# Kernel optimization log

Measured on AMD Instinct MI355X. Metric: run time of the kernel, lower is better.

Reference implementation:

```python
import jax, jax.numpy as jnp
import numpy as np

DT = 0.1
ROUTER_BLOCKS = 64
REPEAT = 64
IN_SIZE = 2048
HIDDEN = 4096
NNZ_W = int(IN_SIZE * HIDDEN * 0.01)   # 83886
NNZ_R = int(HIDDEN * HIDDEN * 0.01)    # 167772
BATCH = 512


def sparse_linear(x, rows, cols, vals, bias, out_features):
    """Edge-list sparse matmul: out[b, cols[e]] += x[b, rows[e]] * vals[e].
    Equivalent to torch.addmm(bias, x, W_csr) with W built from COO (coalesce
    sums duplicates; scatter-add does the same)."""
    contrib = x[:, rows] * vals  # [B, nnz]
    out = jnp.zeros((x.shape[0], out_features), x.dtype).at[:, cols].add(contrib)
    return out + bias


def setup_inputs() -> dict:
    key = jax.random.key(0)
    ks = jax.random.split(key, 20)
    inp = {}
    inp["x"] = jax.random.normal(ks[0], (BATCH, IN_SIZE), jnp.float32)
    inp["h_prev"] = jax.random.normal(ks[1], (BATCH, HIDDEN), jnp.float32)
    inp["gate"] = jax.random.uniform(ks[2], (BATCH, 1), jnp.float32)
    # SparseLinear params (init scale 1/sqrt(in_features), bias zeros)
    inp["W_vals"] = jax.random.normal(ks[3], (NNZ_W,), jnp.float32) / np.sqrt(IN_SIZE).astype(np.float32)
    inp["W_bias"] = jnp.zeros((HIDDEN,), jnp.float32)
    inp["R_vals"] = jax.random.normal(ks[4], (NNZ_R,), jnp.float32) / np.sqrt(HIDDEN).astype(np.float32)
    inp["R_bias"] = jnp.zeros((HIDDEN,), jnp.float32)
    inp["P_vals"] = jax.random.normal(ks[5], (NNZ_R,), jnp.float32) / np.sqrt(HIDDEN).astype(np.float32)
    inp["P_bias"] = jnp.zeros((HIDDEN,), jnp.float32)
    inp["router_w"] = jax.random.normal(ks[6], (ROUTER_BLOCKS, IN_SIZE), jnp.float32) / np.sqrt(IN_SIZE).astype(np.float32)
    inp["router_b"] = jnp.zeros((ROUTER_BLOCKS,), jnp.float32)
    # tau ~ U(0.1, 0.5) per TAU_CONCEPT_RANGE
    inp["tau"] = jax.random.uniform(ks[7], (HIDDEN,), jnp.float32) * 0.4 + 0.1
    # edge lists (int constants)
    inp["W_rows"] = jax.random.randint(ks[8], (NNZ_W,), 0, IN_SIZE, jnp.int32)
    inp["W_cols"] = jax.random.randint(ks[9], (NNZ_W,), 0, HIDDEN, jnp.int32)
    inp["R_rows"] = jax.random.randint(ks[10], (NNZ_R,), 0, HIDDEN, jnp.int32)
    inp["R_cols"] = jax.random.randint(ks[11], (NNZ_R,), 0, HIDDEN, jnp.int32)
    inp["P_rows"] = jax.random.randint(ks[12], (NNZ_R,), 0, HIDDEN, jnp.int32)
    inp["P_cols"] = jax.random.randint(ks[13], (NNZ_R,), 0, HIDDEN, jnp.int32)
    return inp


def reference(x, h_prev, gate, W_vals, W_bias, R_vals, R_bias, P_vals, P_bias,
              router_w, router_b, tau, W_rows, W_cols, R_rows, R_cols, P_rows, P_cols):
    r_gate = jax.nn.sigmoid(x @ router_w.T + router_b)            # [B, 64]
    mask = jnp.repeat(r_gate, REPEAT, axis=1)[:, :HIDDEN]          # [B, hidden]
    sensory = sparse_linear(x, W_rows, W_cols, W_vals, W_bias, HIDDEN) * mask
    rec = sparse_linear(h_prev, R_rows, R_cols, R_vals, R_bias, HIDDEN)
    target = jnp.tanh(sensory + rec)
    h_new = h_prev + gate * (target - h_prev) * (DT / tau)
    pred = sparse_linear(h_new, P_rows, P_cols, P_vals, P_bias, HIDDEN)
    return (h_new, pred)
```

## Files before the change

kernel.cpp:

```cpp
#include <hip/hip_runtime.h>
#include <math.h>

namespace {

constexpr int B     = 512;
constexpr int IN    = 2048;
constexpr int HID   = 4096;
constexpr int NNZ_W = 83886;
constexpr int NNZ_R = 167772;
constexpr int NTOT  = NNZ_W + 2 * NNZ_R;
constexpr int NCOLS = 3 * HID;
constexpr int SLOT  = 128;
constexpr float DT  = 0.1f;

struct ushort4_t { unsigned short x, y, z, w; };

__device__ __forceinline__ float bf2f(unsigned short u) {
  return __uint_as_float((unsigned int)u << 16);
}
__device__ __forceinline__ unsigned short f2bf(float f) {
  unsigned int u = __float_as_uint(f);
  u += 0x7FFFu + ((u >> 16) & 1u);
  return (unsigned short)(u >> 16);
}

__global__ void prep_k(const float* __restrict__ x, unsigned short* __restrict__ xTb,
                       const float* __restrict__ h, float* __restrict__ hT,
                       unsigned short* __restrict__ hTb,
                       const float* __restrict__ rw, const float* __restrict__ rb,
                       float* __restrict__ rgT, int* __restrict__ cnt) {
  __shared__ float sh[4 * IN];
  const int blk = blockIdx.x;
  const int tid = threadIdx.x;

  if (blk < 768) {
    const bool isX = blk < 256;
    const float* src; int C, tb;
    if (isX) { src = x; C = IN;  tb = blk; }
    else     { src = h; C = HID; tb = blk - 256; }
    const int tx_n = C / 64;
    const int bx = (tb % tx_n) * 64;
    const int by = (tb / tx_n) * 64;
    const int tx = tid & 63;
    const int ty = tid >> 6;
    for (int i = ty; i < 64; i += 8)
      sh[i * 65 + tx] = src[(size_t)(by + i) * C + bx + tx];
    __syncthreads();
    for (int i = ty; i < 64; i += 8) {
      const float v = sh[tx * 65 + i];
      const size_t di = (size_t)(bx + i) * B + by + tx;
      if (isX) xTb[di] = f2bf(v);
      else     { hT[di] = v; hTb[di] = f2bf(v); }
    }
  } else if (blk < 896) {
    const int b0 = (blk - 768) * 4;
    for (int k = tid; k < 4 * IN; k += 512) sh[k] = x[(size_t)b0 * IN + k];
    __syncthreads();
    const int wave = tid >> 6;
    const int lane = tid & 63;
#pragma unroll
    for (int j = 0; j < 8; ++j) {
      const int o = wave * 8 + j;
      const float* w = rw + (size_t)o * IN;
      float s0 = 0.f, s1 = 0.f, s2 = 0.f, s3 = 0.f;
      for (int i = 0; i < IN / 64; ++i) {
        const float wv = w[lane + 64 * i];
        s0 += sh[0 * IN + lane + 64 * i] * wv;
        s1 += sh[1 * IN + lane + 64 * i] * wv;
        s2 += sh[2 * IN + lane + 64 * i] * wv;
        s3 += sh[3 * IN + lane + 64 * i] * wv;
      }
#pragma unroll
      for (int d = 1; d < 64; d <<= 1) {
        s0 += __shfl_xor(s0, d);
        s1 += __shfl_xor(s1, d);
        s2 += __shfl_xor(s2, d);
        s3 += __shfl_xor(s3, d);
      }
      if (lane == 0) {
        const float bias = rb[o];
        rgT[o * B + b0 + 0] = 1.f / (1.f + expf(-(s0 + bias)));
        rgT[o * B + b0 + 1] = 1.f / (1.f + expf(-(s1 + bias)));
        rgT[o * B + b0 + 2] = 1.f / (1.f + expf(-(s2 + bias)));
        rgT[o * B + b0 + 3] = 1.f / (1.f + expf(-(s3 + bias)));
      }
    }
  } else {
    const int i = (blk - 896) * 512 + tid;
    if (i < NCOLS) cnt[i] = 0;
  }
}

__global__ void slotscat_k(const int* __restrict__ Wc, const int* __restrict__ Rc,
                           const int* __restrict__ Pc, const int* __restrict__ Wr,
                           const int* __restrict__ Rr, const int* __restrict__ Pr,
                           const float* __restrict__ Wv, const float* __restrict__ Rv,
                           const float* __restrict__ Pv, int* __restrict__ cnt,
                           float2* __restrict__ packed) {
  const int i = blockIdx.x * blockDim.x + threadIdx.x;
  if (i >= NTOT) return;
  int gc, r; float v;
  if (i < NNZ_W)              { gc = Wc[i];                 r = Wr[i]; v = Wv[i]; }
  else if (i < NNZ_W + NNZ_R) { int j = i - NNZ_W;          gc = HID + Rc[j];     r = Rr[j]; v = Rv[j]; }
  else                        { int j = i - NNZ_W - NNZ_R; gc = 2 * HID + Pc[j]; r = Pr[j]; v = Pv[j]; }
  const int p = atomicAdd(&cnt[gc], 1);
  packed[(size_t)gc * SLOT + p] = make_float2(v, __int_as_float(r));
}

__device__ __forceinline__ float4 gather_col_bf(const unsigned short* __restrict__ srcb,
                                                const float2* __restrict__ packed,
                                                int gc, int n, int boff, float bias) {
  float4 acc = make_float4(bias, bias, bias, bias);
  const float2* ep = packed + (size_t)gc * SLOT;
  int i = 0;
  for (; i + 8 <= n; i += 8) {
    float2 e[8]; ushort4_t s[8];
#pragma unroll
    for (int j = 0; j < 8; ++j) e[j] = ep[i + j];
#pragma unroll
    for (int j = 0; j < 8; ++j)
      s[j] = *(const ushort4_t*)(srcb + (size_t)__float_as_int(e[j].y) * B + boff);
#pragma unroll
    for (int j = 0; j < 8; ++j) {
      acc.x += e[j].x * bf2f(s[j].x);
      acc.y += e[j].x * bf2f(s[j].y);
      acc.z += e[j].x * bf2f(s[j].z);
      acc.w += e[j].x * bf2f(s[j].w);
    }
  }
  for (; i < n; ++i) {
    const float2 e = ep[i];
    const ushort4_t s = *(const ushort4_t*)(srcb + (size_t)__float_as_int(e.y) * B + boff);
    acc.x += e.x * bf2f(s.x);
    acc.y += e.x * bf2f(s.y);
    acc.z += e.x * bf2f(s.z);
    acc.w += e.x * bf2f(s.w);
  }
  return acc;
}

__device__ __forceinline__ void col_chunk(int blk, int wave, int& c, int& boff, int lane) {
  const int p = blk & 7;
  const int chunk = p >> 2;
  const int cgrp = ((p & 3) << 8) | (blk >> 3);
  c = cgrp * 4 + wave;
  boff = chunk * 256 + lane * 4;
}

__global__ void fused_gc_k(const unsigned short* __restrict__ xTb,
                           const unsigned short* __restrict__ hTb,
                           const float* __restrict__ hT,
                           const float2* __restrict__ packed, const int* __restrict__ cnt,
                           const float* __restrict__ rgT,
                           const float* __restrict__ gate, const float* __restrict__ tau,
                           const float* __restrict__ wb, const float* __restrict__ rb,
                           float* __restrict__ hnT, unsigned short* __restrict__ hnb) {
  int c, boff;
  col_chunk(blockIdx.x, threadIdx.x >> 6, c, boff, threadIdx.x & 63);

  const float4 sens = gather_col_bf(xTb, packed, c, cnt[c], boff, wb[c]);
  const float4 rec  = gather_col_bf(hTb, packed, HID + c, cnt[HID + c], boff, rb[c]);

  const float4 m  = *(const float4*)(rgT + (size_t)(c >> 6) * B + boff);
  const float4 g  = *(const float4*)(gate + boff);
  const float4 hp = *(const float4*)(hT + (size_t)c * B + boff);
  const float k = DT / tau[c];
  float4 hn;
  hn.x = hp.x + g.x * (tanhf(sens.x * m.x + rec.x) - hp.x) * k;
  hn.y = hp.y + g.y * (tanhf(sens.y * m.y + rec.y) - hp.y) * k;
  hn.z = hp.z + g.z * (tanhf(sens.z * m.z + rec.z) - hp.z) * k;
  hn.w = hp.w + g.w * (tanhf(sens.w * m.w + rec.w) - hp.w) * k;
  *(float4*)(hnT + (size_t)c * B + boff) = hn;
  ushort4_t hb;
  hb.x = f2bf(hn.x); hb.y = f2bf(hn.y); hb.z = f2bf(hn.z); hb.w = f2bf(hn.w);
  *(ushort4_t*)(hnb + (size_t)c * B + boff) = hb;
}

__global__ void pred_k(const unsigned short* __restrict__ hnb,
                       const float2* __restrict__ packed, const int* __restrict__ cnt,
                       const float* __restrict__ pb, float* __restrict__ predT) {
  int c, boff;
  col_chunk(blockIdx.x, threadIdx.x >> 6, c, boff, threadIdx.x & 63);
  const float4 p = gather_col_bf(hnb, packed, 2 * HID + c, cnt[2 * HID + c], boff, pb[c]);
  *(float4*)(predT + (size_t)c * B + boff) = p;
}

__global__ void transpose_out_k(const float* __restrict__ sA, float* __restrict__ dA,
                                int tilesA, const float* __restrict__ sB,
                                float* __restrict__ dB) {
  __shared__ float t[64][65];
  int tb = blockIdx.x;
  const float* src; float* dst;
  if (tb < tilesA) { src = sA; dst = dA; }
  else             { tb -= tilesA; src = sB; dst = dB; }
  const int tx_n = B / 64;
  const int bx = (tb % tx_n) * 64;
  const int by = (tb / tx_n) * 64;
  const int tx = threadIdx.x & 63;
  const int ty = threadIdx.x >> 6;
  for (int i = ty; i < 64; i += 8)
    t[i][tx] = src[(size_t)(by + i) * B + bx + tx];
  __syncthreads();
  for (int i = ty; i < 64; i += 8)
    dst[(size_t)(bx + i) * HID + by + tx] = t[tx][i];
}

}

extern "C" void kernel_launch(void* const* d_in, const int* in_sizes, int n_in,
                              void* d_out, int out_size, void* d_ws, size_t ws_size,
                              hipStream_t stream) {
  const float* x        = (const float*)d_in[0];
  const float* h_prev   = (const float*)d_in[1];
  const float* gate     = (const float*)d_in[2];
  const float* W_vals   = (const float*)d_in[3];
  const float* W_bias   = (const float*)d_in[4];
  const float* R_vals   = (const float*)d_in[5];
  const float* R_bias   = (const float*)d_in[6];
  const float* P_vals   = (const float*)d_in[7];
  const float* P_bias   = (const float*)d_in[8];
  const float* router_w = (const float*)d_in[9];
  const float* router_b = (const float*)d_in[10];
  const float* tau      = (const float*)d_in[11];
  const int* W_rows = (const int*)d_in[12];
  const int* W_cols = (const int*)d_in[13];
  const int* R_rows = (const int*)d_in[14];
  const int* R_cols = (const int*)d_in[15];
  const int* P_rows = (const int*)d_in[16];
  const int* P_cols = (const int*)d_in[17];

  float* ws = (float*)d_ws;
  unsigned short* xTb = (unsigned short*)ws;
  float*  hT     = ws + (size_t)IN * B / 2;
  unsigned short* hTb = (unsigned short*)(hT + (size_t)HID * B);
  float*  rgT    = (float*)(hTb + (size_t)HID * B);
  float*  hnT    = rgT + 64 * B;
  unsigned short* hnb = (unsigned short*)(hnT + (size_t)HID * B);
  float2* packed = (float2*)(hnb + (size_t)HID * B);
  int*    cnt    = (int*)(packed + (size_t)NCOLS * SLOT);
  float*  predT  = ws;

  float* out_h = (float*)d_out;
  float* out_p = out_h + (size_t)B * HID;

  prep_k<<<920, 512, 0, stream>>>(x, xTb, h_prev, hT, hTb,
                                  router_w, router_b, rgT, cnt);

  slotscat_k<<<(NTOT + 255) / 256, 256, 0, stream>>>(W_cols, R_cols, P_cols,
                                                     W_rows, R_rows, P_rows,
                                                     W_vals, R_vals, P_vals,
                                                     cnt, packed);

  fused_gc_k<<<2048, 256, 0, stream>>>(xTb, hTb, hT, packed, cnt, rgT,
                                       gate, tau, W_bias, R_bias, hnT, hnb);

  pred_k<<<2048, 256, 0, stream>>>(hnb, packed, cnt, P_bias, predT);

  transpose_out_k<<<1024, 512, 0, stream>>>(hnT, out_h, 512, predT, out_p);
}
```

Baseline: 114.8 us.

## Overlap h transpose with pred gather and use nontemporal loads/stores

Moves the output transpose of h_new into the pred gather kernel as extra blocks, so it runs alongside the pred sparse gather instead of after it. The pred transpose becomes its own small kernel. Streaming loads and stores throughout (index lists, packed edges, hT, hnT, outputs) are marked nontemporal to reduce cache pollution. Nontemporal hints on the packed edge list, which both gathers reuse, may cost cache hits.

```diff
diff --git a/kernel.cpp b/kernel.cpp
--- a/kernel.cpp
+++ b/kernel.cpp
@@ -12,6 +12,9 @@
 constexpr int NCOLS = 3 * HID;
 constexpr int SLOT  = 128;
 constexpr float DT  = 0.1f;
+
+typedef float f4 __attribute__((ext_vector_type(4)));
+typedef float f2 __attribute__((ext_vector_type(2)));
 
 struct ushort4_t { unsigned short x, y, z, w; };
 
@@ -44,13 +47,13 @@
     const int tx = tid & 63;
     const int ty = tid >> 6;
     for (int i = ty; i < 64; i += 8)
-      sh[i * 65 + tx] = src[(size_t)(by + i) * C + bx + tx];
+      sh[i * 65 + tx] = __builtin_nontemporal_load(&src[(size_t)(by + i) * C + bx + tx]);
     __syncthreads();
     for (int i = ty; i < 64; i += 8) {
       const float v = sh[tx * 65 + i];
       const size_t di = (size_t)(bx + i) * B + by + tx;
       if (isX) xTb[di] = f2bf(v);
-      else     { hT[di] = v; hTb[di] = f2bf(v); }
+      else     { __builtin_nontemporal_store(v, &hT[di]); hTb[di] = f2bf(v); }
     }
   } else if (blk < 896) {
     const int b0 = (blk - 768) * 4;
@@ -100,23 +103,36 @@
   const int i = blockIdx.x * blockDim.x + threadIdx.x;
   if (i >= NTOT) return;
   int gc, r; float v;
-  if (i < NNZ_W)              { gc = Wc[i];                 r = Wr[i]; v = Wv[i]; }
-  else if (i < NNZ_W + NNZ_R) { int j = i - NNZ_W;          gc = HID + Rc[j];     r = Rr[j]; v = Rv[j]; }
-  else                        { int j = i - NNZ_W - NNZ_R; gc = 2 * HID + Pc[j]; r = Pr[j]; v = Pv[j]; }
+  if (i < NNZ_W) {
+    gc = __builtin_nontemporal_load(&Wc[i]);
+    r  = __builtin_nontemporal_load(&Wr[i]);
+    v  = __builtin_nontemporal_load(&Wv[i]);
+  } else if (i < NNZ_W + NNZ_R) {
+    const int j = i - NNZ_W;
+    gc = HID + __builtin_nontemporal_load(&Rc[j]);
+    r  = __builtin_nontemporal_load(&Rr[j]);
+    v  = __builtin_nontemporal_load(&Rv[j]);
+  } else {
+    const int j = i - NNZ_W - NNZ_R;
+    gc = 2 * HID + __builtin_nontemporal_load(&Pc[j]);
+    r  = __builtin_nontemporal_load(&Pr[j]);
+    v  = __builtin_nontemporal_load(&Pv[j]);
+  }
   const int p = atomicAdd(&cnt[gc], 1);
-  packed[(size_t)gc * SLOT + p] = make_float2(v, __int_as_float(r));
-}
-
-__device__ __forceinline__ float4 gather_col_bf(const unsigned short* __restrict__ srcb,
-                                                const float2* __restrict__ packed,
-                                                int gc, int n, int boff, float bias) {
-  float4 acc = make_float4(bias, bias, bias, bias);
-  const float2* ep = packed + (size_t)gc * SLOT;
+  f2 e; e.x = v; e.y = __int_as_float(r);
+  __builtin_nontemporal_store(e, (f2*)&packed[(size_t)gc * SLOT + p]);
+}
+
+__device__ __forceinline__ f4 gather_col_bf(const unsigned short* __restrict__ srcb,
+                                            const float2* __restrict__ packed,
+                                            int gc, int n, int boff, float bias) {
+  f4 acc; acc.x = bias; acc.y = bias; acc.z = bias; acc.w = bias;
+  const f2* ep = (const f2*)(packed + (size_t)gc * SLOT);
   int i = 0;
   for (; i + 8 <= n; i += 8) {
-    float2 e[8]; ushort4_t s[8];
-#pragma unroll
-    for (int j = 0; j < 8; ++j) e[j] = ep[i + j];
+    f2 e[8]; ushort4_t s[8];
+#pragma unroll
+    for (int j = 0; j < 8; ++j) e[j] = __builtin_nontemporal_load(ep + i + j);
 #pragma unroll
     for (int j = 0; j < 8; ++j)
       s[j] = *(const ushort4_t*)(srcb + (size_t)__float_as_int(e[j].y) * B + boff);
@@ -129,7 +145,7 @@
     }
   }
   for (; i < n; ++i) {
-    const float2 e = ep[i];
+    const f2 e = __builtin_nontemporal_load(ep + i);
     const ushort4_t s = *(const ushort4_t*)(srcb + (size_t)__float_as_int(e.y) * B + boff);
     acc.x += e.x * bf2f(s.x);
     acc.y += e.x * bf2f(s.y);
@@ -158,51 +174,63 @@
   int c, boff;
   col_chunk(blockIdx.x, threadIdx.x >> 6, c, boff, threadIdx.x & 63);
 
-  const float4 sens = gather_col_bf(xTb, packed, c, cnt[c], boff, wb[c]);
-  const float4 rec  = gather_col_bf(hTb, packed, HID + c, cnt[HID + c], boff, rb[c]);
-
-  const float4 m  = *(const float4*)(rgT + (size_t)(c >> 6) * B + boff);
-  const float4 g  = *(const float4*)(gate + boff);
-  const float4 hp = *(const float4*)(hT + (size_t)c * B + boff);
+  const f4 sens = gather_col_bf(xTb, packed, c, cnt[c], boff, wb[c]);
+  const f4 rec  = gather_col_bf(hTb, packed, HID + c, cnt[HID + c], boff, rb[c]);
+
+  const f4 m  = *(const f4*)(rgT + (size_t)(c >> 6) * B + boff);
+  const f4 g  = *(const f4*)(gate + boff);
+  const f4 hp = __builtin_nontemporal_load((const f4*)(hT + (size_t)c * B + boff));
   const float k = DT / tau[c];
-  float4 hn;
+  f4 hn;
   hn.x = hp.x + g.x * (tanhf(sens.x * m.x + rec.x) - hp.x) * k;
   hn.y = hp.y + g.y * (tanhf(sens.y * m.y + rec.y) - hp.y) * k;
   hn.z = hp.z + g.z * (tanhf(sens.z * m.z + rec.z) - hp.z) * k;
   hn.w = hp.w + g.w * (tanhf(sens.w * m.w + rec.w) - hp.w) * k;
-  *(float4*)(hnT + (size_t)c * B + boff) = hn;
+  __builtin_nontemporal_store(hn, (f4*)(hnT + (size_t)c * B + boff));
   ushort4_t hb;
   hb.x = f2bf(hn.x); hb.y = f2bf(hn.y); hb.z = f2bf(hn.z); hb.w = f2bf(hn.w);
   *(ushort4_t*)(hnb + (size_t)c * B + boff) = hb;
 }
 
-__global__ void pred_k(const unsigned short* __restrict__ hnb,
-                       const float2* __restrict__ packed, const int* __restrict__ cnt,
-                       const float* __restrict__ pb, float* __restrict__ predT) {
-  int c, boff;
-  col_chunk(blockIdx.x, threadIdx.x >> 6, c, boff, threadIdx.x & 63);
-  const float4 p = gather_col_bf(hnb, packed, 2 * HID + c, cnt[2 * HID + c], boff, pb[c]);
-  *(float4*)(predT + (size_t)c * B + boff) = p;
-}
-
-__global__ void transpose_out_k(const float* __restrict__ sA, float* __restrict__ dA,
-                                int tilesA, const float* __restrict__ sB,
-                                float* __restrict__ dB) {
+__global__ void pred_tr_k(const unsigned short* __restrict__ hnb,
+                          const float2* __restrict__ packed, const int* __restrict__ cnt,
+                          const float* __restrict__ pb, float* __restrict__ predT,
+                          const float* __restrict__ hnT, float* __restrict__ out_h) {
   __shared__ float t[64][65];
-  int tb = blockIdx.x;
-  const float* src; float* dst;
-  if (tb < tilesA) { src = sA; dst = dA; }
-  else             { tb -= tilesA; src = sB; dst = dB; }
+  const int blk = blockIdx.x;
+  if (blk < 2048) {
+    int c, boff;
+    col_chunk(blk, threadIdx.x >> 6, c, boff, threadIdx.x & 63);
+    const f4 p = gather_col_bf(hnb, packed, 2 * HID + c, cnt[2 * HID + c], boff, pb[c]);
+    __builtin_nontemporal_store(p, (f4*)(predT + (size_t)c * B + boff));
+  } else {
+    const int tb = blk - 2048;
+    const int tx_n = B / 64;
+    const int bx = (tb % tx_n) * 64;
+    const int by = (tb / tx_n) * 64;
+    const int tx = threadIdx.x & 63;
+    const int ty = threadIdx.x >> 6;
+    for (int i = ty; i < 64; i += 4)
+      t[i][tx] = __builtin_nontemporal_load(&hnT[(size_t)(by + i) * B + bx + tx]);
+    __syncthreads();
+    for (int i = ty; i < 64; i += 4)
+      __builtin_nontemporal_store(t[tx][i], &out_h[(size_t)(bx + i) * HID + by + tx]);
+  }
+}
+
+__global__ void transpose_p_k(const float* __restrict__ predT, float* __restrict__ out_p) {
+  __shared__ float t[64][65];
+  const int tb = blockIdx.x;
   const int tx_n = B / 64;
   const int bx = (tb % tx_n) * 64;
   const int by = (tb / tx_n) * 64;
   const int tx = threadIdx.x & 63;
   const int ty = threadIdx.x >> 6;
-  for (int i = ty; i < 64; i += 8)
-    t[i][tx] = src[(size_t)(by + i) * B + bx + tx];
+  for (int i = ty; i < 64; i += 4)
+    t[i][tx] = __builtin_nontemporal_load(&predT[(size_t)(by + i) * B + bx + tx]);
   __syncthreads();
-  for (int i = ty; i < 64; i += 8)
-    dst[(size_t)(bx + i) * HID + by + tx] = t[tx][i];
+  for (int i = ty; i < 64; i += 4)
+    __builtin_nontemporal_store(t[tx][i], &out_p[(size_t)(bx + i) * HID + by + tx]);
 }
 
 }
@@ -254,7 +282,7 @@
   fused_gc_k<<<2048, 256, 0, stream>>>(xTb, hTb, hT, packed, cnt, rgT,
                                        gate, tau, W_bias, R_bias, hnT, hnb);
 
-  pred_k<<<2048, 256, 0, stream>>>(hnb, packed, cnt, P_bias, predT);
-
-  transpose_out_k<<<1024, 512, 0, stream>>>(hnT, out_h, 512, predT, out_p);
-}
+  pred_tr_k<<<2560, 256, 0, stream>>>(hnb, packed, cnt, P_bias, predT, hnT, out_h);
+
+  transpose_p_k<<<512, 256, 0, stream>>>(predT, out_p);
+}
```

After: 140.6 us. 1.23x slower.
